# Kernel optimization log

Measured on AMD Instinct MI355X. Metric: run time of the kernel, lower is better.

The kernel has to match this reference:

```python
import jax, jax.numpy as jnp
import numpy as np

NUM_CLASSES = 80
NUM_ANCHORS = 5
ANCHORS = np.array([1.3221, 1.73145, 3.19275, 4.00944, 5.05587, 8.09892,
                    9.47112, 4.84053, 11.2364, 10.0071], dtype=np.float32).reshape(NUM_ANCHORS, 2)
COORD_SCALE = 1.0
NOOBJECT_SCALE = 1.0
OBJECT_SCALE = 5.0
CLASS_SCALE = 1.0
SIL_THRESH = 0.6
MAX_T = 50  # max ground-truth boxes per image
NB, NH, NW = 32, 38, 38


def bbox_iou(b1, b2):
    """IoU for center-format boxes (..., 4) = (cx, cy, w, h); broadcastable.
    Matches darknet bbox_ious with x1y1x2y2=False (zero IoU if no overlap)."""
    mx = jnp.minimum(b1[..., 0] - b1[..., 2] / 2, b2[..., 0] - b2[..., 2] / 2)
    Mx = jnp.maximum(b1[..., 0] + b1[..., 2] / 2, b2[..., 0] + b2[..., 2] / 2)
    my = jnp.minimum(b1[..., 1] - b1[..., 3] / 2, b2[..., 1] - b2[..., 3] / 2)
    My = jnp.maximum(b1[..., 1] + b1[..., 3] / 2, b2[..., 1] + b2[..., 3] / 2)
    cw = b1[..., 2] + b2[..., 2] - (Mx - mx)
    ch = b1[..., 3] + b2[..., 3] - (My - my)
    inter = jnp.where((cw > 0) & (ch > 0), cw * ch, 0.0)
    union = b1[..., 2] * b1[..., 3] + b2[..., 2] * b2[..., 3] - inter
    return inter / jnp.maximum(union, 1e-12)


def setup_inputs() -> dict:
    key = jax.random.key(0)
    k1, k2, k3 = jax.random.split(key, 3)
    output = jax.random.normal(k1, (NB, NUM_ANCHORS * (5 + NUM_CLASSES), NH, NW), dtype=jnp.float32)
    # target rows: 50 boxes x (cls, x, y, w, h), normalized coords in (0,1)
    target = jax.random.uniform(k2, (NB, MAX_T * 5), dtype=jnp.float32, minval=0.02, maxval=0.98)
    features = jax.random.normal(k3, (NB, 512, NH, NW), dtype=jnp.float32)
    return {"output": output, "target": target, "features": features}


def _region_loss(output, target):
    nB, _, nH, nW = output.shape
    nA, nC = NUM_ANCHORS, NUM_CLASSES
    anchors = jnp.asarray(ANCHORS)
    sg = jax.lax.stop_gradient

    out5 = output.reshape(nB, nA, 5 + nC, nH, nW)
    x = jax.nn.sigmoid(out5[:, :, 0])
    y = jax.nn.sigmoid(out5[:, :, 1])
    w = out5[:, :, 2]
    h = out5[:, :, 3]
    conf = jax.nn.sigmoid(out5[:, :, 4])
    cls = jnp.transpose(out5[:, :, 5:], (0, 1, 3, 4, 2))  # [nB,nA,nH,nW,nC]

    # predicted boxes in grid units (detached, as pred_boxes uses .data in torch)
    grid_x = jnp.arange(nW, dtype=output.dtype)
    grid_y = jnp.arange(nH, dtype=output.dtype)
    px = sg(x) + grid_x[None, None, None, :]
    py = sg(y) + grid_y[None, None, :, None]
    pw = jnp.exp(sg(w)) * anchors[None, :, 0, None, None]
    ph = jnp.exp(sg(h)) * anchors[None, :, 1, None, None]
    pred_boxes = jnp.stack([px, py, pw, ph], axis=-1)  # [nB,nA,nH,nW,4]

    tgt = sg(target).reshape(nB, MAX_T, 5)
    gx = tgt[..., 1] * nW
    gy = tgt[..., 2] * nH
    gw = tgt[..., 3] * nW
    gh = tgt[..., 4] * nH
    # original loop breaks at first target x == 0 -> valid prefix mask
    valid = jnp.cumprod((tgt[..., 1] != 0).astype(jnp.int32), axis=1).astype(bool)

    # ---- conf_mask silencing: max IoU of every predicted box vs any GT ----
    gt_boxes = jnp.stack([gx, gy, gw, gh], axis=-1)  # [nB,50,4]
    pb_flat = pred_boxes.reshape(nB, 1, nA * nH * nW, 4)
    ious = bbox_iou(gt_boxes[:, :, None, :], pb_flat)  # [nB,50,nA*nH*nW]
    max_iou = jnp.where(valid[:, :, None], ious, 0.0).max(axis=1).reshape(nB, nA, nH, nW)
    conf_mask = jnp.where(max_iou > SIL_THRESH, 0.0, NOOBJECT_SCALE).astype(output.dtype)

    # ---- seen < 12800 warm-up branch (self.seen = 0, anchor_step = 2) ----
    shp = (nB, nA, nH, nW)
    tx = jnp.full(shp, 0.5, output.dtype)
    ty = jnp.full(shp, 0.5, output.dtype)
    tw = jnp.zeros(shp, output.dtype)
    th = jnp.zeros(shp, output.dtype)
    coord_mask = jnp.ones(shp, output.dtype)
    cls_mask = jnp.zeros(shp, output.dtype)
    tconf = jnp.zeros(shp, output.dtype)
    tcls = jnp.zeros(shp, jnp.int32)

    # ---- best anchor per GT (IoU of wh-only boxes; argmax keeps first max,
    #      matching the strict '>' update in the loop) ----
    zeros = jnp.zeros_like(gw)
    gt_wh = jnp.stack([zeros, zeros, gw, gh], axis=-1)[:, :, None, :]  # [nB,50,1,4]
    anc_wh = jnp.concatenate([jnp.zeros_like(anchors), anchors], axis=-1)[None, None]  # [1,1,nA,4]
    best_n = jnp.argmax(bbox_iou(gt_wh, anc_wh), axis=-1)  # [nB,50]

    gi = jnp.clip(jnp.floor(gx).astype(jnp.int32), 0, nW - 1)
    gj = jnp.clip(jnp.floor(gy).astype(jnp.int32), 0, nH - 1)

    b_idx = jnp.arange(nB)[:, None]
    pbox = pred_boxes[b_idx, best_n, gj, gi]  # [nB,50,4]
    iou_gt = bbox_iou(gt_boxes, pbox)  # [nB,50]

    tx_val = gx - gi.astype(output.dtype)
    ty_val = gy - gj.astype(output.dtype)
    tw_val = jnp.log(jnp.maximum(gw, 1e-12) / anchors[best_n, 0])
    th_val = jnp.log(jnp.maximum(gh, 1e-12) / anchors[best_n, 1])
    cls_val = tgt[..., 0].astype(jnp.int32)

    bi = jnp.arange(nB)

    def step(carry, t):
        coord_m, conf_m, cls_m, tx, ty, tw, th, tconf, tcls = carry
        bn = best_n[:, t]
        j = gj[:, t]
        i = gi[:, t]
        v = valid[:, t]

        def upd(arr, val):
            # indices are distinct within one step (one GT per batch element)
            old = arr[bi, bn, j, i]
            return arr.at[bi, bn, j, i].set(jnp.where(v, val, old))

        coord_m = upd(coord_m, 1.0)
        cls_m = upd(cls_m, 1.0)
        conf_m = upd(conf_m, OBJECT_SCALE)
        tx = upd(tx, tx_val[:, t])
        ty = upd(ty, ty_val[:, t])
        tw = upd(tw, tw_val[:, t])
        th = upd(th, th_val[:, t])
        tconf = upd(tconf, iou_gt[:, t])
        tcls = upd(tcls, cls_val[:, t])
        return (coord_m, conf_m, cls_m, tx, ty, tw, th, tconf, tcls), None

    init = (coord_mask, conf_mask, cls_mask, tx, ty, tw, th, tconf, tcls)
    (coord_mask, conf_mask, cls_mask, tx, ty, tw, th, tconf, tcls), _ = jax.lax.scan(
        step, init, jnp.arange(MAX_T))

    conf_mask = jnp.sqrt(conf_mask)

    loss_x = COORD_SCALE * jnp.sum((x * coord_mask - tx * coord_mask) ** 2) / 2.0
    loss_y = COORD_SCALE * jnp.sum((y * coord_mask - ty * coord_mask) ** 2) / 2.0
    loss_w = COORD_SCALE * jnp.sum((w * coord_mask - tw * coord_mask) ** 2) / 2.0
    loss_h = COORD_SCALE * jnp.sum((h * coord_mask - th * coord_mask) ** 2) / 2.0
    loss_conf = jnp.sum((conf * conf_mask - tconf * conf_mask) ** 2) / 2.0

    # sum-reduced cross entropy over cells where cls_mask == 1
    logp = jax.nn.log_softmax(cls, axis=-1)
    picked = jnp.take_along_axis(logp, tcls[..., None], axis=-1)[..., 0]
    loss_cls = -CLASS_SCALE * jnp.sum(cls_mask * picked)

    return loss_x + loss_y + loss_w + loss_h + loss_conf + loss_cls


def reference(output, target, features):
    # `features` feeds the truncated adversarial-defense tail of the original
    # forward; the detection region loss below is the complete surviving math.
    return _region_loss(output, target)
```

## Files before the change

kernel.cpp:

```cpp
#include <hip/hip_runtime.h>
#include <math.h>

#define NB 32
#define NA 5
#define NC 80
#define NH 38
#define NW 38
#define MAXT 50
#define CELLS (NH * NW)
#define CH (5 + NC)
#define NSLICE 29
#define THREADS 256
#define NWAVES (THREADS / 64)

__device__ float4 g_box[NB][MAXT];
__device__ float  g_thr[NB][MAXT];
__device__ int4   g_tgt[NB][MAXT];
__device__ float  g_corr[NB];

__device__ __forceinline__ float sigmoidf_(float v) {
    return 1.0f / (1.0f + expf(-v));
}

__device__ __forceinline__ float bbox_iou_(float ax, float ay, float aw, float ah,
                                           float bx, float by, float bw, float bh) {
    float mx = fminf(ax - aw * 0.5f, bx - bw * 0.5f);
    float Mx = fmaxf(ax + aw * 0.5f, bx + bw * 0.5f);
    float my = fminf(ay - ah * 0.5f, by - bh * 0.5f);
    float My = fmaxf(ay + ah * 0.5f, by + bh * 0.5f);
    float cw = aw + bw - (Mx - mx);
    float ch = ah + bh - (My - my);
    float inter = (cw > 0.0f && ch > 0.0f) ? cw * ch : 0.0f;
    float uni = aw * ah + bw * bh - inter;
    return inter / fmaxf(uni, 1e-12f);
}

__device__ __constant__ float c_anchors[10] = {
    1.3221f, 1.73145f, 3.19275f, 4.00944f, 5.05587f,
    8.09892f, 9.47112f, 4.84053f, 11.2364f, 10.0071f};

__global__ __launch_bounds__(64) void region_prep(const float* __restrict__ out,
                                                  const float* __restrict__ tgt,
                                                  float* __restrict__ loss) {
    const int b = blockIdx.x;
    const int t = threadIdx.x;
    __shared__ float4 s_box[MAXT];
    __shared__ float  s_thr[MAXT];
    __shared__ int    s_key[64];

    float t0 = 0.f, t1 = 0.f, gx = 0.f, gy = 0.f, gw = 0.f, gh = 0.f;
    const bool isrec = (t < MAXT);
    if (isrec) {
        const float* tp = tgt + (long)b * (MAXT * 5) + t * 5;
        t0 = tp[0];
        t1 = tp[1];
        gx = t1 * NW;
        gy = tp[2] * NH;
        gw = tp[3] * NW;
        gh = tp[4] * NH;
    }
    unsigned long long nz = __ballot(isrec && (t1 != 0.0f));
    bool valid = isrec && (((~nz) & ((2ULL << t) - 1ULL)) == 0ULL);

    int bn = 0;
    float best = -1.0f;
    for (int a = 0; a < NA; ++a) {
        float aw = c_anchors[2 * a], ah = c_anchors[2 * a + 1];
        float inter = fminf(gw, aw) * fminf(gh, ah);
        float uni = gw * gh + aw * ah - inter;
        float iou = inter / fmaxf(uni, 1e-12f);
        if (iou > best) { best = iou; bn = a; }
    }
    int gi = (int)floorf(gx); gi = gi < 0 ? 0 : (gi > NW - 1 ? NW - 1 : gi);
    int gj = (int)floorf(gy); gj = gj < 0 ? 0 : (gj > NH - 1 ? NH - 1 : gj);
    int key = valid ? (bn * CELLS + gj * NW + gi) : -1;
    s_key[t] = key;

    float4 box;
    float thr;
    if (valid) {
        box.x = gx - gw * 0.5f; box.y = gy - gh * 0.5f;
        box.z = gx + gw * 0.5f; box.w = gy + gh * 0.5f;
        thr = 0.375f * (gw * gh);
    } else {
        box.x = box.y = box.z = box.w = 0.0f;
        thr = 3e38f;
    }
    if (isrec) { s_box[t] = box; s_thr[t] = thr; }
    __syncthreads();

    bool winner = valid;
    if (winner) {
        for (int u = t + 1; u < MAXT; ++u)
            if (s_key[u] == key) { winner = false; break; }
    }

    float corr = 0.0f;
    if (winner) {
        float aw = c_anchors[2 * bn], ah = c_anchors[2 * bn + 1];
        long base = (((long)(b * NA + bn)) * CH) * CELLS + gj * NW + gi;
        float xr = out[base];
        float yr = out[base + CELLS];
        float wr = out[base + 2 * CELLS];
        float hr = out[base + 3 * CELLS];
        float cr = out[base + 4 * CELLS];
        float sx = sigmoidf_(xr), sy = sigmoidf_(yr), sc = sigmoidf_(cr);
        float px = sx + (float)gi, py = sy + (float)gj;
        float pw = expf(wr) * aw, ph = expf(hr) * ah;
        float iou_gt = bbox_iou_(gx, gy, gw, gh, px, py, pw, ph);

        float px1 = px - pw * 0.5f, px2 = px + pw * 0.5f;
        float py1 = py - ph * 0.5f, py2 = py + ph * 0.5f;
        float pthr = 0.375f * (pw * ph);
        bool hit = false;
        for (int u = 0; u < MAXT; ++u) {
            float4 rb = s_box[u];
            float ow = fminf(px2, rb.z) - fmaxf(px1, rb.x);
            float oh = fminf(py2, rb.w) - fmaxf(py1, rb.y);
            ow = fmaxf(ow, 0.0f);
            oh = fmaxf(oh, 0.0f);
            hit = hit | (ow * oh > pthr + s_thr[u]);
        }
        float h01 = hit ? 0.0f : 1.0f;

        float txv = gx - (float)gi, tyv = gy - (float)gj;
        float twv = logf(fmaxf(gw, 1e-12f) / aw);
        float thv = logf(fmaxf(gh, 1e-12f) / ah);
        float dsc = sc - iou_gt;
        corr = 0.5f * ((sx - txv) * (sx - txv) - (sx - 0.5f) * (sx - 0.5f)
                     + (sy - tyv) * (sy - tyv) - (sy - 0.5f) * (sy - 0.5f)
                     + (wr - twv) * (wr - twv) - wr * wr
                     + (hr - thv) * (hr - thv) - hr * hr)
             + 0.5f * (5.0f * dsc * dsc - h01 * sc * sc);
    }

    if (isrec) {
        g_box[b][t] = box;
        g_thr[b][t] = thr;
        int cls = (int)t0; cls = cls < 0 ? 0 : (cls > NC - 1 ? NC - 1 : cls);
        int4 ti;
        ti.x = winner ? 1 : 0;
        ti.y = (bn * CH + 5) * CELLS + gj * NW + gi;
        ti.z = cls;
        ti.w = 0;
        g_tgt[b][t] = ti;
    }
    for (int off = 32; off > 0; off >>= 1) corr += __shfl_down(corr, off);
    if (t == 0) {
        g_corr[b] = corr;
        if (b == 0) loss[0] = 0.0f;
    }
}

__global__ __launch_bounds__(THREADS) void region_main(const float* __restrict__ out,
                                                       float* __restrict__ loss) {
    const int bx = blockIdx.x;
    const int b = blockIdx.y;
    const int tid = threadIdx.x;
    const int wid = tid >> 6;
    const int lane = tid & 63;
    __shared__ float4 s_box[MAXT];
    __shared__ float  s_thr[MAXT];
    __shared__ float  s_wpart[NWAVES];

    if (tid < MAXT) {
        s_box[tid] = g_box[b][tid];
        s_thr[tid] = g_thr[b][tid];
    }

    const int idx0 = bx * THREADS + tid;
    int idx = idx0 < NA * CELLS ? idx0 : NA * CELLS - 1;
    const int a = idx / CELLS;
    const int r = idx - a * CELLS;
    const int j = r / NW;
    const int i = r - j * NW;

    const long base = (((long)(b * NA + a)) * CH) * CELLS + r;
    const float xr = out[base];
    const float yr = out[base + CELLS];
    const float wr = out[base + 2 * CELLS];
    const float hr = out[base + 3 * CELLS];
    const float cr = out[base + 4 * CELLS];

    const float sx = sigmoidf_(xr), sy = sigmoidf_(yr), sc = sigmoidf_(cr);
    const float px = sx + (float)i, py = sy + (float)j;
    const float pw = expf(wr) * c_anchors[2 * a];
    const float ph = expf(hr) * c_anchors[2 * a + 1];
    const float px1 = px - pw * 0.5f, px2 = px + pw * 0.5f;
    const float py1 = py - ph * 0.5f, py2 = py + ph * 0.5f;
    const float pthr = 0.375f * (pw * ph);

    __syncthreads();

    bool hit = false;
    #pragma unroll
    for (int u = 0; u < MAXT; ++u) {
        float4 rb = s_box[u];
        float ow = fminf(px2, rb.z) - fmaxf(px1, rb.x);
        float oh = fminf(py2, rb.w) - fmaxf(py1, rb.y);
        ow = fmaxf(ow, 0.0f);
        oh = fmaxf(oh, 0.0f);
        hit = hit | (ow * oh > pthr + s_thr[u]);
    }
    float dx = sx - 0.5f, dy = sy - 0.5f;
    float cellsum = 0.5f * (dx * dx + dy * dy + wr * wr + hr * hr)
                  + (hit ? 0.0f : 0.5f * sc * sc);
    if (idx0 >= NA * CELLS) cellsum = 0.0f;

    float closs = 0.0f;
    const int gwave = __builtin_amdgcn_readfirstlane(bx * NWAVES + wid);
    if (gwave < MAXT) {
        const int4 ti = g_tgt[b][gwave];
        if (ti.x) {
            const float* cp = out + (long)b * (NA * CH * CELLS) + ti.y;
            float v0 = cp[(long)lane * CELLS];
            float v1 = (lane < NC - 64) ? cp[(long)(64 + lane) * CELLS] : -INFINITY;
            float m = fmaxf(v0, v1);
            for (int off = 32; off > 0; off >>= 1)
                m = fmaxf(m, __shfl_down(m, off));
            m = __shfl(m, 0);
            float e = expf(v0 - m) + ((lane < NC - 64) ? expf(v1 - m) : 0.0f);
            for (int off = 32; off > 0; off >>= 1)
                e += __shfl_down(e, off);
            if (lane == 0) closs = m + logf(e) - cp[(long)ti.z * CELLS];
        }
    }
    if (bx == 0 && tid == 0) closs += g_corr[b];

    float v = cellsum;
    for (int off = 32; off > 0; off >>= 1) v += __shfl_down(v, off);
    if (lane == 0) s_wpart[wid] = v + closs;
    __syncthreads();
    if (tid == 0) {
        float s = 0.0f;
        for (int w = 0; w < NWAVES; ++w) s += s_wpart[w];
        atomicAdd(loss, s);
    }
}

extern "C" void kernel_launch(void* const* d_in, const int* in_sizes, int n_in,
                              void* d_out, int out_size, void* d_ws, size_t ws_size,
                              hipStream_t stream) {
    const float* output = (const float*)d_in[0];
    const float* target = (const float*)d_in[1];
    float* loss = (float*)d_out;

    region_prep<<<NB, 64, 0, stream>>>(output, target, loss);
    dim3 grid(NSLICE, NB);
    region_main<<<grid, THREADS, 0, stream>>>(output, loss);
}
```

Baseline: 183.7 us.

## Fuse target-prep kernel into main region-loss kernel with last-block reduction

Removes the separate per-image prep kernel. Every block now recomputes the target boxes, anchor matching and duplicate resolution in its first wave, using shuffles instead of a shared-memory scan, and keeps the results in LDS. The winner-cell correction is computed in slice 0, and the final loss is written by the last finishing block through a global counter instead of a pre-zeroed output. This trades one kernel launch and a global round-trip for redundant target work in every block and a persistent global accumulator and counter.

Measured after the change: 195.8 us. +6.5%, slower.

```diff
diff --git a/kernel.cpp b/kernel.cpp
--- a/kernel.cpp
+++ b/kernel.cpp
@@ -12,11 +12,14 @@
 #define NSLICE 29
 #define THREADS 256
 #define NWAVES (THREADS / 64)
-
-__device__ float4 g_box[NB][MAXT];
-__device__ float  g_thr[NB][MAXT];
-__device__ int4   g_tgt[NB][MAXT];
-__device__ float  g_corr[NB];
+#define NBLOCKS (NSLICE * NB)
+
+__device__ float g_accum = 0.0f;
+__device__ int   g_cnt   = 0;
+
+__device__ __constant__ float c_anchors[10] = {
+    1.3221f, 1.73145f, 3.19275f, 4.00944f, 5.05587f,
+    8.09892f, 9.47112f, 4.84053f, 11.2364f, 10.0071f};
 
 __device__ __forceinline__ float sigmoidf_(float v) {
     return 1.0f / (1.0f + expf(-v));
@@ -35,138 +38,41 @@
     return inter / fmaxf(uni, 1e-12f);
 }
 
-__device__ __constant__ float c_anchors[10] = {
-    1.3221f, 1.73145f, 3.19275f, 4.00944f, 5.05587f,
-    8.09892f, 9.47112f, 4.84053f, 11.2364f, 10.0071f};
-
-__global__ __launch_bounds__(64) void region_prep(const float* __restrict__ out,
-                                                  const float* __restrict__ tgt,
-                                                  float* __restrict__ loss) {
-    const int b = blockIdx.x;
-    const int t = threadIdx.x;
-    __shared__ float4 s_box[MAXT];
-    __shared__ float  s_thr[MAXT];
-    __shared__ int    s_key[64];
-
-    float t0 = 0.f, t1 = 0.f, gx = 0.f, gy = 0.f, gw = 0.f, gh = 0.f;
-    const bool isrec = (t < MAXT);
-    if (isrec) {
-        const float* tp = tgt + (long)b * (MAXT * 5) + t * 5;
-        t0 = tp[0];
-        t1 = tp[1];
-        gx = t1 * NW;
-        gy = tp[2] * NH;
-        gw = tp[3] * NW;
-        gh = tp[4] * NH;
-    }
-    unsigned long long nz = __ballot(isrec && (t1 != 0.0f));
-    bool valid = isrec && (((~nz) & ((2ULL << t) - 1ULL)) == 0ULL);
-
-    int bn = 0;
-    float best = -1.0f;
-    for (int a = 0; a < NA; ++a) {
-        float aw = c_anchors[2 * a], ah = c_anchors[2 * a + 1];
-        float inter = fminf(gw, aw) * fminf(gh, ah);
-        float uni = gw * gh + aw * ah - inter;
-        float iou = inter / fmaxf(uni, 1e-12f);
-        if (iou > best) { best = iou; bn = a; }
-    }
-    int gi = (int)floorf(gx); gi = gi < 0 ? 0 : (gi > NW - 1 ? NW - 1 : gi);
-    int gj = (int)floorf(gy); gj = gj < 0 ? 0 : (gj > NH - 1 ? NH - 1 : gj);
-    int key = valid ? (bn * CELLS + gj * NW + gi) : -1;
-    s_key[t] = key;
-
-    float4 box;
-    float thr;
-    if (valid) {
-        box.x = gx - gw * 0.5f; box.y = gy - gh * 0.5f;
-        box.z = gx + gw * 0.5f; box.w = gy + gh * 0.5f;
-        thr = 0.375f * (gw * gh);
-    } else {
-        box.x = box.y = box.z = box.w = 0.0f;
-        thr = 3e38f;
-    }
-    if (isrec) { s_box[t] = box; s_thr[t] = thr; }
-    __syncthreads();
-
-    bool winner = valid;
-    if (winner) {
-        for (int u = t + 1; u < MAXT; ++u)
-            if (s_key[u] == key) { winner = false; break; }
-    }
-
-    float corr = 0.0f;
-    if (winner) {
-        float aw = c_anchors[2 * bn], ah = c_anchors[2 * bn + 1];
-        long base = (((long)(b * NA + bn)) * CH) * CELLS + gj * NW + gi;
-        float xr = out[base];
-        float yr = out[base + CELLS];
-        float wr = out[base + 2 * CELLS];
-        float hr = out[base + 3 * CELLS];
-        float cr = out[base + 4 * CELLS];
-        float sx = sigmoidf_(xr), sy = sigmoidf_(yr), sc = sigmoidf_(cr);
-        float px = sx + (float)gi, py = sy + (float)gj;
-        float pw = expf(wr) * aw, ph = expf(hr) * ah;
-        float iou_gt = bbox_iou_(gx, gy, gw, gh, px, py, pw, ph);
-
-        float px1 = px - pw * 0.5f, px2 = px + pw * 0.5f;
-        float py1 = py - ph * 0.5f, py2 = py + ph * 0.5f;
-        float pthr = 0.375f * (pw * ph);
-        bool hit = false;
-        for (int u = 0; u < MAXT; ++u) {
-            float4 rb = s_box[u];
-            float ow = fminf(px2, rb.z) - fmaxf(px1, rb.x);
-            float oh = fminf(py2, rb.w) - fmaxf(py1, rb.y);
-            ow = fmaxf(ow, 0.0f);
-            oh = fmaxf(oh, 0.0f);
-            hit = hit | (ow * oh > pthr + s_thr[u]);
-        }
-        float h01 = hit ? 0.0f : 1.0f;
-
-        float txv = gx - (float)gi, tyv = gy - (float)gj;
-        float twv = logf(fmaxf(gw, 1e-12f) / aw);
-        float thv = logf(fmaxf(gh, 1e-12f) / ah);
-        float dsc = sc - iou_gt;
-        corr = 0.5f * ((sx - txv) * (sx - txv) - (sx - 0.5f) * (sx - 0.5f)
-                     + (sy - tyv) * (sy - tyv) - (sy - 0.5f) * (sy - 0.5f)
-                     + (wr - twv) * (wr - twv) - wr * wr
-                     + (hr - thv) * (hr - thv) - hr * hr)
-             + 0.5f * (5.0f * dsc * dsc - h01 * sc * sc);
-    }
-
-    if (isrec) {
-        g_box[b][t] = box;
-        g_thr[b][t] = thr;
-        int cls = (int)t0; cls = cls < 0 ? 0 : (cls > NC - 1 ? NC - 1 : cls);
-        int4 ti;
-        ti.x = winner ? 1 : 0;
-        ti.y = (bn * CH + 5) * CELLS + gj * NW + gi;
-        ti.z = cls;
-        ti.w = 0;
-        g_tgt[b][t] = ti;
-    }
-    for (int off = 32; off > 0; off >>= 1) corr += __shfl_down(corr, off);
-    if (t == 0) {
-        g_corr[b] = corr;
-        if (b == 0) loss[0] = 0.0f;
-    }
-}
-
-__global__ __launch_bounds__(THREADS) void region_main(const float* __restrict__ out,
-                                                       float* __restrict__ loss) {
+__device__ __forceinline__ bool hit50_(float px, float py, float pw, float ph,
+                                       const float4* __restrict__ sb,
+                                       const float* __restrict__ st) {
+    float x1 = px - pw * 0.5f, x2 = px + pw * 0.5f;
+    float y1 = py - ph * 0.5f, y2 = py + ph * 0.5f;
+    float pthr = 0.375f * (pw * ph);
+    bool hit = false;
+    #pragma unroll
+    for (int u = 0; u < MAXT; ++u) {
+        float4 rb = sb[u];
+        float ow = fminf(x2, rb.z) - fmaxf(x1, rb.x);
+        float oh = fminf(y2, rb.w) - fmaxf(y1, rb.y);
+        ow = fmaxf(ow, 0.0f);
+        oh = fmaxf(oh, 0.0f);
+        hit = hit | (ow * oh > pthr + st[u]);
+    }
+    return hit;
+}
+
+__global__ __launch_bounds__(THREADS) void region_fused(const float* __restrict__ out,
+                                                        const float* __restrict__ tgt,
+                                                        float* __restrict__ loss) {
     const int bx = blockIdx.x;
     const int b = blockIdx.y;
     const int tid = threadIdx.x;
     const int wid = tid >> 6;
     const int lane = tid & 63;
+
     __shared__ float4 s_box[MAXT];
     __shared__ float  s_thr[MAXT];
+    __shared__ int    s_win[MAXT];
+    __shared__ int    s_off[MAXT];
+    __shared__ int    s_cls[MAXT];
     __shared__ float  s_wpart[NWAVES];
-
-    if (tid < MAXT) {
-        s_box[tid] = g_box[b][tid];
-        s_thr[tid] = g_thr[b][tid];
-    }
+    __shared__ int    s_flag;
 
     const int idx0 = bx * THREADS + tid;
     int idx = idx0 < NA * CELLS ? idx0 : NA * CELLS - 1;
@@ -174,7 +80,6 @@
     const int r = idx - a * CELLS;
     const int j = r / NW;
     const int i = r - j * NW;
-
     const long base = (((long)(b * NA + a)) * CH) * CELLS + r;
     const float xr = out[base];
     const float yr = out[base + CELLS];
@@ -182,50 +87,124 @@
     const float hr = out[base + 3 * CELLS];
     const float cr = out[base + 4 * CELLS];
 
+    float gx = 0.f, gy = 0.f, gw = 0.f, gh = 0.f;
+    float rxr = 0.f, ryr = 0.f, rwr = 0.f, rhr = 0.f, rcr = 0.f;
+    int bn = 0, gi = 0, gj = 0;
+    bool winner = false;
+    if (wid == 0) {
+        const bool isrec = (lane < MAXT);
+        float t0 = 0.f, t1 = 0.f;
+        if (isrec) {
+            const float* tp = tgt + (long)b * (MAXT * 5) + lane * 5;
+            t0 = tp[0];
+            t1 = tp[1];
+            gx = t1 * NW;
+            gy = tp[2] * NH;
+            gw = tp[3] * NW;
+            gh = tp[4] * NH;
+        }
+        unsigned long long nz = __ballot(isrec && (t1 != 0.0f));
+        bool valid = isrec && (((~nz) & ((2ULL << lane) - 1ULL)) == 0ULL);
+
+        float best = -1.0f;
+        for (int aa = 0; aa < NA; ++aa) {
+            float aw = c_anchors[2 * aa], ah = c_anchors[2 * aa + 1];
+            float inter = fminf(gw, aw) * fminf(gh, ah);
+            float uni = gw * gh + aw * ah - inter;
+            float iou = inter / fmaxf(uni, 1e-12f);
+            if (iou > best) { best = iou; bn = aa; }
+        }
+        gi = (int)floorf(gx); gi = gi < 0 ? 0 : (gi > NW - 1 ? NW - 1 : gi);
+        gj = (int)floorf(gy); gj = gj < 0 ? 0 : (gj > NH - 1 ? NH - 1 : gj);
+        int key = valid ? (bn * CELLS + gj * NW + gi) : -1;
+
+        unsigned long long eq = 0ULL;
+        for (int u = 0; u < MAXT; ++u) {
+            int ku = __shfl(key, u);
+            eq |= (unsigned long long)(ku == key) << u;
+        }
+        winner = valid && ((eq & ~((2ULL << lane) - 1ULL)) == 0ULL);
+
+        float4 box;
+        float thr;
+        if (valid) {
+            box.x = gx - gw * 0.5f; box.y = gy - gh * 0.5f;
+            box.z = gx + gw * 0.5f; box.w = gy + gh * 0.5f;
+            thr = 0.375f * (gw * gh);
+        } else {
+            box.x = box.y = box.z = box.w = 0.0f;
+            thr = 3e38f;
+        }
+        if (isrec) {
+            s_box[lane] = box;
+            s_thr[lane] = thr;
+            s_win[lane] = winner ? 1 : 0;
+            int cls = (int)t0; cls = cls < 0 ? 0 : (cls > NC - 1 ? NC - 1 : cls);
+            s_cls[lane] = cls;
+            s_off[lane] = (bn * CH + 5) * CELLS + gj * NW + gi;
+        }
+        if (bx == 0 && winner) {
+            long rb = (((long)(b * NA + bn)) * CH) * CELLS + gj * NW + gi;
+            rxr = out[rb];
+            ryr = out[rb + CELLS];
+            rwr = out[rb + 2 * CELLS];
+            rhr = out[rb + 3 * CELLS];
+            rcr = out[rb + 4 * CELLS];
+        }
+    }
+    __syncthreads();
+
+    const int gwave = bx * NWAVES + wid;
+    float v0 = -INFINITY, v1 = -INFINITY, vc = 0.0f;
+    bool doClass = false;
+    if (gwave < MAXT && s_win[gwave]) {
+        doClass = true;
+        const float* cp = out + (long)b * (NA * CH * CELLS) + s_off[gwave];
+        v0 = cp[(long)lane * CELLS];
+        v1 = (lane < NC - 64) ? cp[(long)(64 + lane) * CELLS] : -INFINITY;
+        vc = cp[(long)s_cls[gwave] * CELLS];
+    }
+
     const float sx = sigmoidf_(xr), sy = sigmoidf_(yr), sc = sigmoidf_(cr);
     const float px = sx + (float)i, py = sy + (float)j;
     const float pw = expf(wr) * c_anchors[2 * a];
     const float ph = expf(hr) * c_anchors[2 * a + 1];
-    const float px1 = px - pw * 0.5f, px2 = px + pw * 0.5f;
-    const float py1 = py - ph * 0.5f, py2 = py + ph * 0.5f;
-    const float pthr = 0.375f * (pw * ph);
-
-    __syncthreads();
-
-    bool hit = false;
-    #pragma unroll
-    for (int u = 0; u < MAXT; ++u) {
-        float4 rb = s_box[u];
-        float ow = fminf(px2, rb.z) - fmaxf(px1, rb.x);
-        float oh = fminf(py2, rb.w) - fmaxf(py1, rb.y);
-        ow = fmaxf(ow, 0.0f);
-        oh = fmaxf(oh, 0.0f);
-        hit = hit | (ow * oh > pthr + s_thr[u]);
-    }
+    const bool hit = hit50_(px, py, pw, ph, s_box, s_thr);
     float dx = sx - 0.5f, dy = sy - 0.5f;
     float cellsum = 0.5f * (dx * dx + dy * dy + wr * wr + hr * hr)
                   + (hit ? 0.0f : 0.5f * sc * sc);
     if (idx0 >= NA * CELLS) cellsum = 0.0f;
 
+    if (bx == 0 && wid == 0 && winner) {
+        float aw = c_anchors[2 * bn], ah = c_anchors[2 * bn + 1];
+        float csx = sigmoidf_(rxr), csy = sigmoidf_(ryr), csc = sigmoidf_(rcr);
+        float cpx = csx + (float)gi, cpy = csy + (float)gj;
+        float cpw = expf(rwr) * aw, cph = expf(rhr) * ah;
+        float iou_gt = bbox_iou_(gx, gy, gw, gh, cpx, cpy, cpw, cph);
+        bool rhit = hit50_(cpx, cpy, cpw, cph, s_box, s_thr);
+        float h01 = rhit ? 0.0f : 1.0f;
+        float txv = gx - (float)gi, tyv = gy - (float)gj;
+        float twv = logf(fmaxf(gw, 1e-12f) / aw);
+        float thv = logf(fmaxf(gh, 1e-12f) / ah);
+        float dsc = csc - iou_gt;
+        cellsum += 0.5f * ((csx - txv) * (csx - txv) - (csx - 0.5f) * (csx - 0.5f)
+                         + (csy - tyv) * (csy - tyv) - (csy - 0.5f) * (csy - 0.5f)
+                         + (rwr - twv) * (rwr - twv) - rwr * rwr
+                         + (rhr - thv) * (rhr - thv) - rhr * rhr)
+                 + 0.5f * (5.0f * dsc * dsc - h01 * csc * csc);
+    }
+
     float closs = 0.0f;
-    const int gwave = __builtin_amdgcn_readfirstlane(bx * NWAVES + wid);
-    if (gwave < MAXT) {
-        const int4 ti = g_tgt[b][gwave];
-        if (ti.x) {
-            const float* cp = out + (long)b * (NA * CH * CELLS) + ti.y;
-            float v0 = cp[(long)lane * CELLS];
-            float v1 = (lane < NC - 64) ? cp[(long)(64 + lane) * CELLS] : -INFINITY;
-            float m = fmaxf(v0, v1);
-            for (int off = 32; off > 0; off >>= 1)
-                m = fmaxf(m, __shfl_down(m, off));
-            m = __shfl(m, 0);
-            float e = expf(v0 - m) + ((lane < NC - 64) ? expf(v1 - m) : 0.0f);
-            for (int off = 32; off > 0; off >>= 1)
-                e += __shfl_down(e, off);
-            if (lane == 0) closs = m + logf(e) - cp[(long)ti.z * CELLS];
-        }
-    }
-    if (bx == 0 && tid == 0) closs += g_corr[b];
+    if (doClass) {
+        float m = fmaxf(v0, v1);
+        for (int off = 32; off > 0; off >>= 1)
+            m = fmaxf(m, __shfl_down(m, off));
+        m = __shfl(m, 0);
+        float e = expf(v0 - m) + ((lane < NC - 64) ? expf(v1 - m) : 0.0f);
+        for (int off = 32; off > 0; off >>= 1)
+            e += __shfl_down(e, off);
+        if (lane == 0) closs = m + logf(e) - vc;
+    }
 
     float v = cellsum;
     for (int off = 32; off > 0; off >>= 1) v += __shfl_down(v, off);
@@ -234,7 +213,18 @@
     if (tid == 0) {
         float s = 0.0f;
         for (int w = 0; w < NWAVES; ++w) s += s_wpart[w];
-        atomicAdd(loss, s);
+        atomicAdd(&g_accum, s);
+        __threadfence();
+        int old = atomicAdd(&g_cnt, 1);
+        s_flag = (old == NBLOCKS - 1) ? 1 : 0;
+    }
+    __syncthreads();
+    if (s_flag) {
+        if (tid == 0) {
+            __threadfence();
+            loss[0] = atomicExch(&g_accum, 0.0f);
+            atomicExch(&g_cnt, 0);
+        }
     }
 }
 
@@ -245,7 +235,6 @@
     const float* target = (const float*)d_in[1];
     float* loss = (float*)d_out;
 
-    region_prep<<<NB, 64, 0, stream>>>(output, target, loss);
     dim3 grid(NSLICE, NB);
-    region_main<<<grid, THREADS, 0, stream>>>(output, loss);
-}
+    region_fused<<<grid, THREADS, 0, stream>>>(output, target, loss);
+}
```
